# Kernel optimization log

Hardware: AMD Instinct MI355X
Metric: run time of the kernel (lower is better)

The kernel has to match this reference:

```python
import jax, jax.numpy as jnp
import numpy as np
import math

D_MODEL = 1024
N_HEADS = 16
HEAD_DIM = D_MODEL // N_HEADS
THETA = 10000.0


def _rope(x, cos, sin):
    # x: [b, h, s, head_dim]; cos/sin: [s, head_dim//2]
    xe = x[..., 0::2]
    xo = x[..., 1::2]
    re = xe * cos - xo * sin
    ro = xe * sin + xo * cos
    # interleave back to even/odd layout
    return jnp.stack([re, ro], axis=-1).reshape(x.shape)


def setup_inputs() -> dict:
    key = jax.random.key(0)
    k1, k2, k3, k4, k5 = jax.random.split(key, 5)
    std = math.sqrt(2.0 / (D_MODEL + D_MODEL))
    x = jax.random.normal(k1, (2, 2048, D_MODEL), dtype=jnp.float32)
    Wq = jax.random.normal(k2, (D_MODEL, D_MODEL), dtype=jnp.float32) * std
    Wk = jax.random.normal(k3, (D_MODEL, D_MODEL), dtype=jnp.float32) * std
    Wv = jax.random.normal(k4, (D_MODEL, D_MODEL), dtype=jnp.float32) * std
    Wo = jax.random.normal(k5, (D_MODEL, D_MODEL), dtype=jnp.float32) * (std / math.sqrt(2))
    return {"x": x, "Wq": Wq, "Wk": Wk, "Wv": Wv, "Wo": Wo}


def reference(x, Wq, Wk, Wv, Wo):
    b, s, d = x.shape
    h, hd = N_HEADS, HEAD_DIM
    # projections: einsum 'batch seq d_in, d_model d_in -> batch seq d_model' == x @ W.T
    def proj(W):
        y = jnp.einsum('bsd,md->bsm', x, W)
        return y.reshape(b, s, h, hd).transpose(0, 2, 1, 3)  # [b, h, s, hd]
    Q, K, V = proj(Wq), proj(Wk), proj(Wv)
    # RoPE with default positions = arange(seq)
    freqs = 1.0 / (THETA ** (jnp.arange(0, hd, 2, dtype=jnp.float32) / hd))
    angles = jnp.arange(s, dtype=jnp.float32)[:, None] * freqs[None, :]  # [s, hd//2]
    cos, sin = jnp.cos(angles), jnp.sin(angles)
    Q = _rope(Q, cos, sin)
    K = _rope(K, cos, sin)
    # naive causal attention
    scores = jnp.einsum('bhqd,bhkd->bhqk', Q, K) / math.sqrt(hd)
    causal = jnp.tril(jnp.ones((s, s), dtype=bool))
    scores = jnp.where(causal, scores, -jnp.inf)
    attn = jax.nn.softmax(scores, axis=-1)
    out = jnp.einsum('bhqk,bhkd->bhqd', attn, V)
    out = out.transpose(0, 2, 1, 3).reshape(b, s, d)
    return jnp.einsum('bsd,md->bsm', out, Wo)
```

## Files before the change

kernel.cpp:

```cpp
#include <hip/hip_runtime.h>
#include <stdint.h>
#include <stddef.h>

typedef __bf16 bf16;
typedef __bf16 bf16x8 __attribute__((ext_vector_type(8)));
typedef __bf16 bf16x4 __attribute__((ext_vector_type(4)));
typedef short short4v __attribute__((ext_vector_type(4)));
typedef float f32x4 __attribute__((ext_vector_type(4)));

#define GAS __attribute__((address_space(1)))
#define LAS __attribute__((address_space(3)))

__device__ __forceinline__ void async_load16(const void* g, void* l) {
  __builtin_amdgcn_global_load_lds((const GAS void*)g, (LAS void*)l, 16, 0, 0);
}

__device__ __forceinline__ f32x4 mfma16(bf16x4 a, bf16x4 b, f32x4 c) {
#if defined(__HIP_DEVICE_COMPILE__)
#if __has_builtin(__builtin_amdgcn_mfma_f32_16x16x16bf16_1k)
  return __builtin_amdgcn_mfma_f32_16x16x16bf16_1k(
      __builtin_bit_cast(short4v, a), __builtin_bit_cast(short4v, b), c, 0, 0, 0);
#else
  f32x4 d;
  asm volatile("v_mfma_f32_16x16x16_bf16 %0, %1, %2, %3"
               : "=v"(d)
               : "v"(a), "v"(b), "v"(c));
  return d;
#endif
#else
  (void)a; (void)b;
  return c;
#endif
}

__global__ __launch_bounds__(256) void cast_all(
    const float* __restrict__ x, const float* __restrict__ Wq,
    const float* __restrict__ Wk, const float* __restrict__ Wv,
    const float* __restrict__ Wo, bf16* __restrict__ Xh,
    bf16* __restrict__ Wqkv, bf16* __restrict__ Woh) {
  int idx = blockIdx.x * 256 + threadIdx.x;
  if (idx < 4194304) {
    Xh[idx] = (bf16)x[idx];
  } else if (idx < 7340032) {
    int j = idx - 4194304;
    if (j < 1048576) {
      Wqkv[j] = (bf16)(Wq[j] * 0.18033688011112042f);
    } else {
      const float* W = (j < 2097152) ? Wk : Wv;
      Wqkv[j] = (bf16)W[j & 1048575];
    }
  } else {
    int j = idx - 7340032;
    Woh[j] = (bf16)Wo[j];
  }
}

__global__ __launch_bounds__(256) void gemm_qkv(
    const bf16* __restrict__ A, const bf16* __restrict__ B,
    bf16* __restrict__ QKV2, bf16* __restrict__ Vt, int K) {
  __shared__ __align__(16) bf16 As[128 * 32];
  __shared__ __align__(16) bf16 Bs[128 * 32];
  const int tid = threadIdx.x;
  const int wave = tid >> 6, lane = tid & 63;
  const int bm = blockIdx.y * 128, bn = blockIdx.x * 128;
  const int wm = (wave >> 1) * 64, wn = (wave & 1) * 64;
  const int lrow = lane >> 2, lk = (lane & 3) * 8;
  const int fr = lane & 15, fk = (lane >> 4) * 8;

  f32x4 acc[4][4] = {};

  for (int kt = 0; kt < K; kt += 32) {
    __syncthreads();
#pragma unroll
    for (int c = 0; c < 2; ++c) {
      const int chunk = wave * 2 + c;
      const bf16* ga = A + (size_t)(bm + chunk * 16 + lrow) * K + kt + lk;
      async_load16(ga, (void*)(As + chunk * 512));
      const bf16* gb = B + (size_t)(bn + chunk * 16 + lrow) * K + kt + lk;
      async_load16(gb, (void*)(Bs + chunk * 512));
    }
    __syncthreads();

    bf16x8 af[4], bfr[4];
#pragma unroll
    for (int i = 0; i < 4; ++i)
      af[i] = *(const bf16x8*)&As[(wm + i * 16 + fr) * 32 + fk];
#pragma unroll
    for (int j = 0; j < 4; ++j)
      bfr[j] = *(const bf16x8*)&Bs[(wn + j * 16 + fr) * 32 + fk];
#pragma unroll
    for (int i = 0; i < 4; ++i)
#pragma unroll
      for (int j = 0; j < 4; ++j)
        acc[i][j] =
            __builtin_amdgcn_mfma_f32_16x16x32_bf16(af[i], bfr[j], acc[i][j], 0, 0, 0);
  }

  const int r0 = (lane >> 4) * 4, cc = lane & 15;
#pragma unroll
  for (int i = 0; i < 4; ++i) {
    const int row0 = bm + wm + i * 16 + r0;
#pragma unroll
    for (int j = 0; j < 4; ++j) {
      const int col = bn + wn + j * 16 + cc;
      if (col < 2048) {
#pragma unroll
        for (int r = 0; r < 4; ++r)
          QKV2[(size_t)(row0 + r) * 2048 + col] = (bf16)acc[i][j][r];
      } else {
        const int v = col - 2048, h = v >> 6, d = v & 63;
        const int b = row0 >> 11, s = row0 & 2047;
        bf16x4 o;
#pragma unroll
        for (int r = 0; r < 4; ++r) o[r] = (bf16)acc[i][j][r];
        *(bf16x4*)&Vt[(((size_t)b * 16 + h) * 64 + d) * 2048 + s] = o;
      }
    }
  }
}

template <typename OutT, int BM, int BN>
__global__ __launch_bounds__(256) void gemm_bt(
    const bf16* __restrict__ A, const bf16* __restrict__ B,
    OutT* __restrict__ C, int M, int N, int K) {
  constexpr int ACH = BM / 16, NCH = (BM + BN) / 16, PW = NCH / 4;
  constexpr int FM = BM / 32, FN = BN / 32;
  __shared__ __align__(16) bf16 As[BM * 32];
  __shared__ __align__(16) bf16 Bs[BN * 32];
  const int tid = threadIdx.x;
  const int wave = tid >> 6, lane = tid & 63;
  const int bm = blockIdx.y * BM, bn = blockIdx.x * BN;
  const int wm = (wave >> 1) * (BM / 2), wn = (wave & 1) * (BN / 2);
  const int lrow = lane >> 2, lk = (lane & 3) * 8;
  const int fr = lane & 15, fk = (lane >> 4) * 8;

  f32x4 acc[FM][FN] = {};

  for (int kt = 0; kt < K; kt += 32) {
    __syncthreads();
#pragma unroll
    for (int c = 0; c < PW; ++c) {
      const int chunk = wave * PW + c;
      if (chunk < ACH) {
        const bf16* ga = A + (size_t)(bm + chunk * 16 + lrow) * K + kt + lk;
        async_load16(ga, (void*)(As + chunk * 512));
      } else {
        const int bc = chunk - ACH;
        const bf16* gb = B + (size_t)(bn + bc * 16 + lrow) * K + kt + lk;
        async_load16(gb, (void*)(Bs + bc * 512));
      }
    }
    __syncthreads();

    bf16x8 af[FM], bfr[FN];
#pragma unroll
    for (int i = 0; i < FM; ++i)
      af[i] = *(const bf16x8*)&As[(wm + i * 16 + fr) * 32 + fk];
#pragma unroll
    for (int j = 0; j < FN; ++j)
      bfr[j] = *(const bf16x8*)&Bs[(wn + j * 16 + fr) * 32 + fk];
#pragma unroll
    for (int i = 0; i < FM; ++i)
#pragma unroll
      for (int j = 0; j < FN; ++j)
        acc[i][j] =
            __builtin_amdgcn_mfma_f32_16x16x32_bf16(af[i], bfr[j], acc[i][j], 0, 0, 0);
  }

  const int r0 = (lane >> 4) * 4, cc = lane & 15;
#pragma unroll
  for (int i = 0; i < FM; ++i)
#pragma unroll
    for (int j = 0; j < FN; ++j)
#pragma unroll
      for (int r = 0; r < 4; ++r)
        C[(size_t)(bm + wm + i * 16 + r0 + r) * N + (bn + wn + j * 16 + cc)] =
            (OutT)acc[i][j][r];
}

__global__ __launch_bounds__(256) void rope_qk(const bf16* __restrict__ QKV2,
                                               bf16* __restrict__ Qh,
                                               bf16* __restrict__ Kh) {
  int idx = blockIdx.x * 256 + threadIdx.x;
  int row = idx >> 10, cp = idx & 1023;
  int col = cp << 1;
  size_t base = (size_t)row * 2048 + col;
  float xe = (float)QKV2[base], xo = (float)QKV2[base + 1];
  int s = row & 2047, b = row >> 11;
  int i = cp & 31;
  float freq = expf((float)i * -0.2878231366242557f);
  float sn, cs;
  sincosf((float)s * freq, &sn, &cs);
  float re = xe * cs - xo * sn;
  float ro = xe * sn + xo * cs;
  int hcol = col & 1023;
  int h = hcol >> 6, d = hcol & 63;
  bf16* dst = (col < 1024 ? Qh : Kh) + ((size_t)(b * 16 + h) * 2048 + s) * 64 + d;
  dst[0] = (bf16)re;
  dst[1] = (bf16)ro;
}

__global__ __launch_bounds__(128, 2) void attn(const bf16* __restrict__ Qh,
                                               const bf16* __restrict__ Kh,
                                               const bf16* __restrict__ Vt,
                                               bf16* __restrict__ Oh) {
  __shared__ __align__(16) bf16 Ks[2][64 * 72];
  __shared__ __align__(16) bf16 Vs[2][64 * 72];
  const int qt = 31 - (int)blockIdx.x;
  const int bh = blockIdx.y;
  const int tid = threadIdx.x, w = tid >> 6, lane = tid & 63;
  const int nlo = lane & 15, g = lane >> 4;
  const int q0 = qt * 64;
  const size_t hq = (size_t)bh * 2048 * 64;
  const bf16* __restrict__ Kp = Kh + hq;
  const bf16* __restrict__ Vp = Vt + hq;

  const int srow = tid >> 1, soff = (tid & 1) * 32;

  bf16x8 aq[2][2];
#pragma unroll
  for (int qb = 0; qb < 2; ++qb)
#pragma unroll
    for (int ks = 0; ks < 2; ++ks)
      aq[qb][ks] = *(const bf16x8*)&Qh[hq +
          (size_t)(q0 + (w * 2 + qb) * 16 + nlo) * 64 + ks * 32 + g * 8];

  bf16x4 ones;
#pragma unroll
  for (int t = 0; t < 4; ++t) ones[t] = (bf16)1.0f;

  f32x4 oacc[2][4] = {};
  f32x4 lacc[2] = {};

  bf16x8 pk[4], pv[4];
#pragma unroll
  for (int c = 0; c < 4; ++c) {
    pk[c] = *(const bf16x8*)&Kp[(size_t)srow * 64 + soff + c * 8];
    pv[c] = *(const bf16x8*)&Vp[(size_t)srow * 2048 + soff + c * 8];
  }

  for (int i = 0; i <= qt; ++i) {
    const int buf = i & 1;
    const int kbase = i * 64;
#pragma unroll
    for (int c = 0; c < 4; ++c) {
      *(bf16x8*)&Ks[buf][srow * 72 + soff + c * 8] = pk[c];
      *(bf16x8*)&Vs[buf][srow * 72 + soff + c * 8] = pv[c];
    }
    __syncthreads();

    if (i < qt) {
      const int kb2 = kbase + 64;
#pragma unroll
      for (int c = 0; c < 4; ++c) {
        pk[c] = *(const bf16x8*)&Kp[(size_t)(kb2 + srow) * 64 + soff + c * 8];
        pv[c] = *(const bf16x8*)&Vp[(size_t)srow * 2048 + kb2 + soff + c * 8];
      }
    }

    f32x4 st[2][4] = {};
#pragma unroll
    for (int ks = 0; ks < 2; ++ks)
#pragma unroll
      for (int ni = 0; ni < 4; ++ni) {
        bf16x8 ak = *(const bf16x8*)&Ks[buf][(ni * 16 + nlo) * 72 + ks * 32 + g * 8];
#pragma unroll
        for (int qb = 0; qb < 2; ++qb)
          st[qb][ni] = __builtin_amdgcn_mfma_f32_16x16x32_bf16(ak, aq[qb][ks],
                                                               st[qb][ni], 0, 0, 0);
      }

    const bool dg = (i == qt);
    bf16x4 p[2][4];
#pragma unroll
    for (int qb = 0; qb < 2; ++qb) {
      const int qg = q0 + (w * 2 + qb) * 16 + nlo;
#pragma unroll
      for (int ni = 0; ni < 4; ++ni) {
        const int kg0 = kbase + ni * 16 + g * 4;
#pragma unroll
        for (int r = 0; r < 4; ++r) {
          float e = __builtin_amdgcn_exp2f(st[qb][ni][r]);
          p[qb][ni][r] = (bf16)((!dg || (kg0 + r <= qg)) ? e : 0.0f);
        }
      }
    }

#pragma unroll
    for (int ni = 0; ni < 4; ++ni) {
      lacc[0] = mfma16(ones, p[0][ni], lacc[0]);
      lacc[1] = mfma16(ones, p[1][ni], lacc[1]);
#pragma unroll
      for (int mi = 0; mi < 4; ++mi) {
        bf16x4 av = *(const bf16x4*)&Vs[buf][(mi * 16 + nlo) * 72 + ni * 16 + g * 4];
        oacc[0][mi] = mfma16(av, p[0][ni], oacc[0][mi]);
        oacc[1][mi] = mfma16(av, p[1][ni], oacc[1][mi]);
      }
    }
  }

  const int b = bh >> 4, h = bh & 15;
#pragma unroll
  for (int qb = 0; qb < 2; ++qb) {
    const int q = q0 + (w * 2 + qb) * 16 + nlo;
    const float inv = 1.0f / lacc[qb][0];
#pragma unroll
    for (int mi = 0; mi < 4; ++mi) {
      bf16x4 o;
#pragma unroll
      for (int r = 0; r < 4; ++r) o[r] = (bf16)(oacc[qb][mi][r] * inv);
      *(bf16x4*)&Oh[((size_t)b * 2048 + q) * 1024 + h * 64 + mi * 16 + g * 4] = o;
    }
  }
}

extern "C" void kernel_launch(void* const* d_in, const int* in_sizes, int n_in,
                              void* d_out, int out_size, void* d_ws, size_t ws_size,
                              hipStream_t stream) {
  (void)in_sizes; (void)n_in; (void)out_size; (void)ws_size;
  const float* x = (const float*)d_in[0];
  const float* Wq = (const float*)d_in[1];
  const float* Wk = (const float*)d_in[2];
  const float* Wv = (const float*)d_in[3];
  const float* Wo = (const float*)d_in[4];
  float* out = (float*)d_out;
  char* ws = (char*)d_ws;

  bf16* Xh   = (bf16*)(ws);
  bf16* Wqkv = (bf16*)(ws + 8388608);
  bf16* Woh  = (bf16*)(ws + 14680064);
  bf16* QKV2 = (bf16*)(ws + 16777216);
  bf16* Qh   = (bf16*)(ws + 33554432);
  bf16* Kh   = (bf16*)(ws + 41943040);
  bf16* Vt   = (bf16*)(ws + 50331648);
  bf16* Oh   = (bf16*)(ws + 58720256);

  cast_all<<<32768, 256, 0, stream>>>(x, Wq, Wk, Wv, Wo, Xh, Wqkv, Woh);
  gemm_qkv<<<dim3(24, 32), 256, 0, stream>>>(Xh, Wqkv, QKV2, Vt, 1024);
  rope_qk<<<16384, 256, 0, stream>>>(QKV2, Qh, Kh);
  attn<<<dim3(32, 32), 128, 0, stream>>>(Qh, Kh, Vt, Oh);
  gemm_bt<float, 128, 64><<<dim3(16, 32), 256, 0, stream>>>(Oh, Woh, out, 4096, 1024, 1024);
}
```

Measured before the change: 208.9 us.

## Split K into head-dim halves and stream it to LDS with async loads

RoPE now writes K in a split layout, with each 32-wide half of the head dimension stored contiguously per head. The attention kernel then fetches K tiles straight into LDS with global_load_lds, skipping the register round trip and the padded LDS layout. The grid is flattened and remapped so that alternate groups of heads walk the causal q-tiles in opposite order, which balances work across blocks. The occupancy hint is dropped and RoPE uses fast intrinsic exp and sincos. The unpadded 32-element LDS rows may cause bank conflicts, and the fast trig loses some accuracy at large angles.

```diff
diff --git a/kernel.cpp b/kernel.cpp
--- a/kernel.cpp
+++ b/kernel.cpp
@@ -180,7 +180,7 @@
 
 __global__ __launch_bounds__(256) void rope_qk(const bf16* __restrict__ QKV2,
                                                bf16* __restrict__ Qh,
-                                               bf16* __restrict__ Kh) {
+                                               bf16* __restrict__ Kh2) {
   int idx = blockIdx.x * 256 + threadIdx.x;
   int row = idx >> 10, cp = idx & 1023;
   int col = cp << 1;
@@ -188,42 +188,52 @@
   float xe = (float)QKV2[base], xo = (float)QKV2[base + 1];
   int s = row & 2047, b = row >> 11;
   int i = cp & 31;
-  float freq = expf((float)i * -0.2878231366242557f);
+  float freq = __expf((float)i * -0.2878231366242557f);
   float sn, cs;
-  sincosf((float)s * freq, &sn, &cs);
+  __sincosf((float)s * freq, &sn, &cs);
   float re = xe * cs - xo * sn;
   float ro = xe * sn + xo * cs;
   int hcol = col & 1023;
   int h = hcol >> 6, d = hcol & 63;
-  bf16* dst = (col < 1024 ? Qh : Kh) + ((size_t)(b * 16 + h) * 2048 + s) * 64 + d;
-  dst[0] = (bf16)re;
-  dst[1] = (bf16)ro;
-}
-
-__global__ __launch_bounds__(128, 2) void attn(const bf16* __restrict__ Qh,
-                                               const bf16* __restrict__ Kh,
-                                               const bf16* __restrict__ Vt,
-                                               bf16* __restrict__ Oh) {
-  __shared__ __align__(16) bf16 Ks[2][64 * 72];
+  int bh = b * 16 + h;
+  if (col < 1024) {
+    bf16* dst = Qh + ((size_t)bh * 2048 + s) * 64 + d;
+    dst[0] = (bf16)re;
+    dst[1] = (bf16)ro;
+  } else {
+    bf16* dst = Kh2 + ((size_t)bh * 2 + (d >> 5)) * 65536 + (size_t)s * 32 + (d & 31);
+    dst[0] = (bf16)re;
+    dst[1] = (bf16)ro;
+  }
+}
+
+__global__ __launch_bounds__(128) void attn(const bf16* __restrict__ Qh,
+                                            const bf16* __restrict__ Kh2,
+                                            const bf16* __restrict__ Vt,
+                                            bf16* __restrict__ Oh) {
+  __shared__ __align__(16) bf16 Ks[2][2 * 64 * 32];
   __shared__ __align__(16) bf16 Vs[2][64 * 72];
-  const int qt = 31 - (int)blockIdx.x;
-  const int bh = blockIdx.y;
+  const int f = blockIdx.x;
+  const int u = f & 255, v = f >> 8;
+  const int qt = (v & 1) ? (31 - (u & 31)) : (u & 31);
+  const int bh = v * 8 + (u >> 5);
   const int tid = threadIdx.x, w = tid >> 6, lane = tid & 63;
   const int nlo = lane & 15, g = lane >> 4;
   const int q0 = qt * 64;
-  const size_t hq = (size_t)bh * 2048 * 64;
-  const bf16* __restrict__ Kp = Kh + hq;
-  const bf16* __restrict__ Vp = Vt + hq;
+  const bf16* __restrict__ Kp = Kh2 + (size_t)bh * 131072;
+  const bf16* __restrict__ Vp = Vt + (size_t)bh * 131072;
+  const bf16* __restrict__ Qp = Qh + (size_t)bh * 131072;
 
   const int srow = tid >> 1, soff = (tid & 1) * 32;
+  const int kkey = lane >> 2, kd = (lane & 3) * 8;
 
   bf16x8 aq[2][2];
 #pragma unroll
   for (int qb = 0; qb < 2; ++qb)
 #pragma unroll
     for (int ks = 0; ks < 2; ++ks)
-      aq[qb][ks] = *(const bf16x8*)&Qh[hq +
-          (size_t)(q0 + (w * 2 + qb) * 16 + nlo) * 64 + ks * 32 + g * 8];
+      aq[qb][ks] = *(const bf16x8*)&Qp[(size_t)(q0 + (w * 2 + qb) * 16 + nlo) * 64 +
+                                       ks * 32 + g * 8];
 
   bf16x4 ones;
 #pragma unroll
@@ -232,30 +242,36 @@
   f32x4 oacc[2][4] = {};
   f32x4 lacc[2] = {};
 
-  bf16x8 pk[4], pv[4];
-#pragma unroll
-  for (int c = 0; c < 4; ++c) {
-    pk[c] = *(const bf16x8*)&Kp[(size_t)srow * 64 + soff + c * 8];
+  bf16x8 pv[4];
+#pragma unroll
+  for (int c = 0; c < 4; ++c)
     pv[c] = *(const bf16x8*)&Vp[(size_t)srow * 2048 + soff + c * 8];
+#pragma unroll
+  for (int jj = 0; jj < 4; ++jj) {
+    const int j = w * 4 + jj, half = j >> 2, key = (j & 3) * 16 + kkey;
+    async_load16(Kp + (size_t)half * 65536 + (size_t)key * 32 + kd,
+                 (void*)(&Ks[0][j * 512]));
   }
 
   for (int i = 0; i <= qt; ++i) {
     const int buf = i & 1;
     const int kbase = i * 64;
 #pragma unroll
-    for (int c = 0; c < 4; ++c) {
-      *(bf16x8*)&Ks[buf][srow * 72 + soff + c * 8] = pk[c];
+    for (int c = 0; c < 4; ++c)
       *(bf16x8*)&Vs[buf][srow * 72 + soff + c * 8] = pv[c];
-    }
     __syncthreads();
 
     if (i < qt) {
       const int kb2 = kbase + 64;
 #pragma unroll
-      for (int c = 0; c < 4; ++c) {
-        pk[c] = *(const bf16x8*)&Kp[(size_t)(kb2 + srow) * 64 + soff + c * 8];
+      for (int jj = 0; jj < 4; ++jj) {
+        const int j = w * 4 + jj, half = j >> 2, key = (j & 3) * 16 + kkey;
+        async_load16(Kp + (size_t)half * 65536 + (size_t)(kb2 + key) * 32 + kd,
+                     (void*)(&Ks[buf ^ 1][j * 512]));
+      }
+#pragma unroll
+      for (int c = 0; c < 4; ++c)
         pv[c] = *(const bf16x8*)&Vp[(size_t)srow * 2048 + kb2 + soff + c * 8];
-      }
     }
 
     f32x4 st[2][4] = {};
@@ -263,7 +279,8 @@
     for (int ks = 0; ks < 2; ++ks)
 #pragma unroll
       for (int ni = 0; ni < 4; ++ni) {
-        bf16x8 ak = *(const bf16x8*)&Ks[buf][(ni * 16 + nlo) * 72 + ks * 32 + g * 8];
+        bf16x8 ak =
+            *(const bf16x8*)&Ks[buf][ks * 2048 + (ni * 16 + nlo) * 32 + g * 8];
 #pragma unroll
         for (int qb = 0; qb < 2; ++qb)
           st[qb][ni] = __builtin_amdgcn_mfma_f32_16x16x32_bf16(ak, aq[qb][ks],
@@ -331,13 +348,13 @@
   bf16* Woh  = (bf16*)(ws + 14680064);
   bf16* QKV2 = (bf16*)(ws + 16777216);
   bf16* Qh   = (bf16*)(ws + 33554432);
-  bf16* Kh   = (bf16*)(ws + 41943040);
+  bf16* Kh2  = (bf16*)(ws + 41943040);
   bf16* Vt   = (bf16*)(ws + 50331648);
   bf16* Oh   = (bf16*)(ws + 58720256);
 
   cast_all<<<32768, 256, 0, stream>>>(x, Wq, Wk, Wv, Wo, Xh, Wqkv, Woh);
   gemm_qkv<<<dim3(24, 32), 256, 0, stream>>>(Xh, Wqkv, QKV2, Vt, 1024);
-  rope_qk<<<16384, 256, 0, stream>>>(QKV2, Qh, Kh);
-  attn<<<dim3(32, 32), 128, 0, stream>>>(Qh, Kh, Vt, Oh);
+  rope_qk<<<16384, 256, 0, stream>>>(QKV2, Qh, Kh2);
+  attn<<<1024, 128, 0, stream>>>(Qh, Kh2, Vt, Oh);
   gemm_bt<float, 128, 64><<<dim3(16, 32), 256, 0, stream>>>(Oh, Woh, out, 4096, 1024, 1024);
 }
```

Result: slower. 213.3 us (+2.1%).

## Split causal KV range across waves in attention and merge partial results

Applied to the files above, without the earlier changes.

The attention kernel now has each block's two waves cover all 64 query rows but split the causal key tiles in half. Each wave loads K fragments straight from global memory into registers, with no LDS staging for K, and keeps a private V buffer in LDS. This removes the per-tile block-wide barrier. Row sums are now kept in registers and reduced with shuffles instead of a ones-MFMA. Wave 1 writes its partial output and sums to LDS scratch, and wave 0 merges them and normalizes. The grid is flattened so that long query tiles launch first. RoPE switches to the fast __expf/__sincosf intrinsics, which trade accuracy at large angles for speed. Risks include more registers for the 4x4 accumulators, direct global K reads, and uneven work between the two waves.

```diff
diff --git a/kernel.cpp b/kernel.cpp
--- a/kernel.cpp
+++ b/kernel.cpp
@@ -188,9 +188,9 @@
   float xe = (float)QKV2[base], xo = (float)QKV2[base + 1];
   int s = row & 2047, b = row >> 11;
   int i = cp & 31;
-  float freq = expf((float)i * -0.2878231366242557f);
+  float freq = __expf((float)i * -0.2878231366242557f);
   float sn, cs;
-  sincosf((float)s * freq, &sn, &cs);
+  __sincosf((float)s * freq, &sn, &cs);
   float re = xe * cs - xo * sn;
   float ro = xe * sn + xo * cs;
   int hcol = col & 1023;
@@ -204,112 +204,132 @@
                                                const bf16* __restrict__ Kh,
                                                const bf16* __restrict__ Vt,
                                                bf16* __restrict__ Oh) {
-  __shared__ __align__(16) bf16 Ks[2][64 * 72];
   __shared__ __align__(16) bf16 Vs[2][64 * 72];
-  const int qt = 31 - (int)blockIdx.x;
-  const int bh = blockIdx.y;
+  __shared__ float scratch[68 * 64];
+  const int f = blockIdx.x;
+  const int qt = 31 - (f >> 5);
+  const int bh = f & 31;
   const int tid = threadIdx.x, w = tid >> 6, lane = tid & 63;
   const int nlo = lane & 15, g = lane >> 4;
   const int q0 = qt * 64;
-  const size_t hq = (size_t)bh * 2048 * 64;
-  const bf16* __restrict__ Kp = Kh + hq;
-  const bf16* __restrict__ Vp = Vt + hq;
-
-  const int srow = tid >> 1, soff = (tid & 1) * 32;
-
-  bf16x8 aq[2][2];
-#pragma unroll
-  for (int qb = 0; qb < 2; ++qb)
+  const bf16* __restrict__ Qp = Qh + (size_t)bh * 131072;
+  const bf16* __restrict__ Kp = Kh + (size_t)bh * 131072;
+  const bf16* __restrict__ Vp = Vt + (size_t)bh * 131072;
+  const int n = qt + 1;
+  const int hf = (n + 1) >> 1;
+  const int t0 = w ? hf : 0;
+  const int cnt = w ? (n - hf) : hf;
+
+  bf16x8 aq[4][2];
+#pragma unroll
+  for (int qb = 0; qb < 4; ++qb)
 #pragma unroll
     for (int ks = 0; ks < 2; ++ks)
-      aq[qb][ks] = *(const bf16x8*)&Qh[hq +
-          (size_t)(q0 + (w * 2 + qb) * 16 + nlo) * 64 + ks * 32 + g * 8];
-
-  bf16x4 ones;
-#pragma unroll
-  for (int t = 0; t < 4; ++t) ones[t] = (bf16)1.0f;
-
-  f32x4 oacc[2][4] = {};
-  f32x4 lacc[2] = {};
-
-  bf16x8 pk[4], pv[4];
-#pragma unroll
-  for (int c = 0; c < 4; ++c) {
-    pk[c] = *(const bf16x8*)&Kp[(size_t)srow * 64 + soff + c * 8];
-    pv[c] = *(const bf16x8*)&Vp[(size_t)srow * 2048 + soff + c * 8];
-  }
-
-  for (int i = 0; i <= qt; ++i) {
-    const int buf = i & 1;
-    const int kbase = i * 64;
-#pragma unroll
-    for (int c = 0; c < 4; ++c) {
-      *(bf16x8*)&Ks[buf][srow * 72 + soff + c * 8] = pk[c];
-      *(bf16x8*)&Vs[buf][srow * 72 + soff + c * 8] = pv[c];
-    }
-    __syncthreads();
-
-    if (i < qt) {
+      aq[qb][ks] =
+          *(const bf16x8*)&Qp[(size_t)(q0 + qb * 16 + nlo) * 64 + ks * 32 + g * 8];
+
+  f32x4 oacc[4][4] = {};
+  float lsum[4] = {0.f, 0.f, 0.f, 0.f};
+
+  const int srow = lane >> 3, soff = (lane & 7) * 8;
+  bf16* __restrict__ Vw = Vs[w];
+
+  bf16x8 pv[8];
+  if (cnt > 0) {
+#pragma unroll
+    for (int c = 0; c < 8; ++c)
+      pv[c] = *(const bf16x8*)&Vp[(size_t)(c * 8 + srow) * 2048 + t0 * 64 + soff];
+  }
+
+  for (int it = 0; it < cnt; ++it) {
+    const int i = t0 + it, kbase = i * 64;
+    bf16x8 pk[4][2];
+#pragma unroll
+    for (int ni = 0; ni < 4; ++ni)
+#pragma unroll
+      for (int ks = 0; ks < 2; ++ks)
+        pk[ni][ks] = *(const bf16x8*)&Kp[(size_t)(kbase + ni * 16 + nlo) * 64 +
+                                         ks * 32 + g * 8];
+#pragma unroll
+    for (int c = 0; c < 8; ++c)
+      *(bf16x8*)&Vw[(c * 8 + srow) * 72 + soff] = pv[c];
+    if (it + 1 < cnt) {
       const int kb2 = kbase + 64;
 #pragma unroll
-      for (int c = 0; c < 4; ++c) {
-        pk[c] = *(const bf16x8*)&Kp[(size_t)(kb2 + srow) * 64 + soff + c * 8];
-        pv[c] = *(const bf16x8*)&Vp[(size_t)srow * 2048 + kb2 + soff + c * 8];
-      }
-    }
-
-    f32x4 st[2][4] = {};
-#pragma unroll
-    for (int ks = 0; ks < 2; ++ks)
-#pragma unroll
-      for (int ni = 0; ni < 4; ++ni) {
-        bf16x8 ak = *(const bf16x8*)&Ks[buf][(ni * 16 + nlo) * 72 + ks * 32 + g * 8];
-#pragma unroll
-        for (int qb = 0; qb < 2; ++qb)
-          st[qb][ni] = __builtin_amdgcn_mfma_f32_16x16x32_bf16(ak, aq[qb][ks],
-                                                               st[qb][ni], 0, 0, 0);
-      }
-
-    const bool dg = (i == qt);
-    bf16x4 p[2][4];
-#pragma unroll
-    for (int qb = 0; qb < 2; ++qb) {
-      const int qg = q0 + (w * 2 + qb) * 16 + nlo;
+      for (int c = 0; c < 8; ++c)
+        pv[c] = *(const bf16x8*)&Vp[(size_t)(c * 8 + srow) * 2048 + kb2 + soff];
+    }
+
+    const bool dg = (i == n - 1);
+    bf16x4 p[4][4];
+#pragma unroll
+    for (int qb = 0; qb < 4; ++qb) {
+      f32x4 st[4] = {};
+#pragma unroll
+      for (int ks = 0; ks < 2; ++ks)
+#pragma unroll
+        for (int ni = 0; ni < 4; ++ni)
+          st[ni] = __builtin_amdgcn_mfma_f32_16x16x32_bf16(pk[ni][ks], aq[qb][ks],
+                                                           st[ni], 0, 0, 0);
+      const int qg = q0 + qb * 16 + nlo;
 #pragma unroll
       for (int ni = 0; ni < 4; ++ni) {
         const int kg0 = kbase + ni * 16 + g * 4;
 #pragma unroll
         for (int r = 0; r < 4; ++r) {
-          float e = __builtin_amdgcn_exp2f(st[qb][ni][r]);
-          p[qb][ni][r] = (bf16)((!dg || (kg0 + r <= qg)) ? e : 0.0f);
+          float e = __builtin_amdgcn_exp2f(st[ni][r]);
+          e = (!dg || (kg0 + r <= qg)) ? e : 0.0f;
+          lsum[qb] += e;
+          p[qb][ni][r] = (bf16)e;
         }
       }
     }
 
 #pragma unroll
-    for (int ni = 0; ni < 4; ++ni) {
-      lacc[0] = mfma16(ones, p[0][ni], lacc[0]);
-      lacc[1] = mfma16(ones, p[1][ni], lacc[1]);
+    for (int ni = 0; ni < 4; ++ni)
 #pragma unroll
       for (int mi = 0; mi < 4; ++mi) {
-        bf16x4 av = *(const bf16x4*)&Vs[buf][(mi * 16 + nlo) * 72 + ni * 16 + g * 4];
-        oacc[0][mi] = mfma16(av, p[0][ni], oacc[0][mi]);
-        oacc[1][mi] = mfma16(av, p[1][ni], oacc[1][mi]);
-      }
-    }
-  }
-
-  const int b = bh >> 4, h = bh & 15;
-#pragma unroll
-  for (int qb = 0; qb < 2; ++qb) {
-    const int q = q0 + (w * 2 + qb) * 16 + nlo;
-    const float inv = 1.0f / lacc[qb][0];
-#pragma unroll
-    for (int mi = 0; mi < 4; ++mi) {
-      bf16x4 o;
-#pragma unroll
-      for (int r = 0; r < 4; ++r) o[r] = (bf16)(oacc[qb][mi][r] * inv);
-      *(bf16x4*)&Oh[((size_t)b * 2048 + q) * 1024 + h * 64 + mi * 16 + g * 4] = o;
+        bf16x4 av = *(const bf16x4*)&Vw[(mi * 16 + nlo) * 72 + ni * 16 + g * 4];
+#pragma unroll
+        for (int qb = 0; qb < 4; ++qb)
+          oacc[qb][mi] = mfma16(av, p[qb][ni], oacc[qb][mi]);
+      }
+  }
+
+#pragma unroll
+  for (int qb = 0; qb < 4; ++qb) {
+    lsum[qb] += __shfl_xor(lsum[qb], 16, 64);
+    lsum[qb] += __shfl_xor(lsum[qb], 32, 64);
+  }
+
+  if (w == 1) {
+#pragma unroll
+    for (int qb = 0; qb < 4; ++qb) {
+#pragma unroll
+      for (int mi = 0; mi < 4; ++mi)
+#pragma unroll
+        for (int r = 0; r < 4; ++r)
+          scratch[(qb * 16 + mi * 4 + r) * 64 + lane] = oacc[qb][mi][r];
+      scratch[(64 + qb) * 64 + lane] = lsum[qb];
+    }
+  }
+  __syncthreads();
+  if (w == 0) {
+    const int b = bh >> 4, hd = bh & 15;
+#pragma unroll
+    for (int qb = 0; qb < 4; ++qb) {
+      const float l = lsum[qb] + scratch[(64 + qb) * 64 + lane];
+      const float inv = 1.0f / l;
+      const int q = q0 + qb * 16 + nlo;
+#pragma unroll
+      for (int mi = 0; mi < 4; ++mi) {
+        bf16x4 o;
+#pragma unroll
+        for (int r = 0; r < 4; ++r)
+          o[r] = (bf16)((oacc[qb][mi][r] +
+                         scratch[(qb * 16 + mi * 4 + r) * 64 + lane]) * inv);
+        *(bf16x4*)&Oh[((size_t)b * 2048 + q) * 1024 + hd * 64 + mi * 16 + g * 4] = o;
+      }
     }
   }
 }
@@ -338,6 +358,6 @@
   cast_all<<<32768, 256, 0, stream>>>(x, Wq, Wk, Wv, Wo, Xh, Wqkv, Woh);
   gemm_qkv<<<dim3(24, 32), 256, 0, stream>>>(Xh, Wqkv, QKV2, Vt, 1024);
   rope_qk<<<16384, 256, 0, stream>>>(QKV2, Qh, Kh);
-  attn<<<dim3(32, 32), 128, 0, stream>>>(Qh, Kh, Vt, Oh);
+  attn<<<1024, 128, 0, stream>>>(Qh, Kh, Vt, Oh);
   gemm_bt<float, 128, 64><<<dim3(16, 32), 256, 0, stream>>>(Oh, Woh, out, 4096, 1024, 1024);
 }
```

New measurement: 204.5 us. -2.1%, faster.
